# Performance work log

Hardware: AMD Instinct MI355X
Metric: run time of the kernel (lower is better)

## Reference

```python
import jax, jax.numpy as jnp
import numpy as np

B, N, DIM = 2, 8192, 3
K = 16            # num_neighbours (dilation=1)
R = 2048          # num_representitives
CIN, CL, COUT = 64, 16, 128
K2 = K * K


def _bn(x, g, b):
    # BatchNorm in eval mode with running_mean=0, running_var=1 -> affine
    return x * g + b


def setup_inputs() -> dict:
    key = jax.random.key(0)
    ks = jax.random.split(key, 24)
    r = lambda i, shape, s=1.0: jax.random.normal(ks[i], shape, jnp.float32) * s
    return {
        "points": r(0, (B, N, DIM)),
        "features": r(1, (B, N, CIN)),
        "lift_w": r(2, (CL, DIM), 0.3), "lift_b": r(3, (CL,), 0.1),
        "bn_lift_g": 1.0 + r(4, (CL,), 0.1), "bn_lift_b": r(5, (CL,), 0.1),
        "t1_w": r(6, (K2, DIM * K), 0.1), "t1_b": r(7, (K2,), 0.1),
        "bn1_g": 1.0 + r(8, (K2,), 0.1), "bn1_b": r(9, (K2,), 0.1),
        "t2_w": r(10, (K2, K2), 0.05), "t2_b": r(11, (K2,), 0.1),
        "bn2_g": 1.0 + r(12, (K2,), 0.1), "bn2_b": r(13, (K2,), 0.1),
        "t3_w": r(14, (K2, K2), 0.05), "t3_b": r(15, (K2,), 0.1),
        "bn3_g": 1.0 + r(16, (K2,), 0.1), "bn3_b": r(17, (K2,), 0.1),
        "conv_w": r(18, (COUT, CIN + CL, K), 0.05), "conv_b": r(19, (COUT,), 0.1),
        "rep_idx": jax.random.permutation(ks[20], N)[:R],
    }


def reference(points, features, lift_w, lift_b, bn_lift_g, bn_lift_b,
              t1_w, t1_b, bn1_g, bn1_b, t2_w, t2_b, bn2_g, bn2_b,
              t3_w, t3_b, bn3_g, bn3_b, conv_w, conv_b, rep_idx):
    b, n, _ = points.shape
    # ---- KNN (squared distance is order-equivalent to torch.cdist) ----
    sq = jnp.sum(points * points, -1)                                   # (b,n)
    d2 = sq[:, :, None] + sq[:, None, :] - 2.0 * jnp.einsum('bnd,bmd->bnm', points, points)
    _, idx = jax.lax.top_k(-d2, K + 1)                                  # (b,n,K+1)
    nn_idx = idx[:, :, 1:]                                              # drop self
    # ---- representative sampling + neighbor gather ----
    rep_pos = points[:, rep_idx]                                        # (b,R,3)
    nb_idx = nn_idx[:, rep_idx]                                         # (b,R,K)
    gather = jax.vmap(lambda arr, i: arr[i])
    nbr_pos = gather(points, nb_idx)                                    # (b,R,K,3)
    nbr_feat = gather(features, nb_idx)                                 # (b,R,K,CIN)
    # ---- X_conv ----
    p = (nbr_pos - rep_pos[:, :, None, :]).reshape(b * R, K, DIM)       # centered
    lifted = jax.nn.relu(_bn(p @ lift_w.T + lift_b, bn_lift_g, bn_lift_b))  # (bR,K,CL)
    feat = jnp.concatenate([lifted, nbr_feat.reshape(b * R, K, CIN)], -1)   # (bR,K,CL+CIN)
    pf = p.reshape(b * R, K * DIM)
    h = jax.nn.relu(_bn(pf @ t1_w.T + t1_b, bn1_g, bn1_b))
    h = jax.nn.relu(_bn(h @ t2_w.T + t2_b, bn2_g, bn2_b))
    T = _bn(h @ t3_w.T + t3_b, bn3_g, bn3_b).reshape(b * R, K, K)       # learned transform
    Tf = jnp.einsum('bij,bjc->bic', T, feat)                            # bmm, (bR,K,C)
    # Conv1d(C, COUT, kernel=K) over length K -> single output position
    out = jnp.einsum('bkc,ock->bo', Tf, conv_w) + conv_b                # (bR,COUT)
    return rep_pos, out.reshape(b, R, COUT)
```

## Files before the change

### kernel.cpp

```cpp
#include <hip/hip_runtime.h>
#include <float.h>

#define Bn 2
#define Nn 8192
#define Rr 2048
#define Kk 16
#define CIN 64
#define CL 16
#define COUT 128
#define K2c 256
#define GT (Bn*Rr)
#define FD (CL+CIN)
#define KC (Kk*FD)
#define MG 4
#define CCAP 192

__global__ __launch_bounds__(256) void prep_kernel(
    const float* __restrict__ t1_w, const float* __restrict__ t2_w,
    const float* __restrict__ t3_w, const float* __restrict__ conv_w,
    const float* __restrict__ points,
    float* __restrict__ t1t, float* __restrict__ t2t,
    float* __restrict__ t3t, float* __restrict__ wp,
    float4* __restrict__ pts4)
{
  int i = blockIdx.x * 256 + threadIdx.x;
  if (i < K2c*48) { int j = i / 48, k = i - j*48; t1t[k*K2c + j] = t1_w[i]; }
  if (i < K2c*K2c) { int j = i >> 8, k = i & 255; t2t[k*K2c + j] = t2_w[i]; t3t[k*K2c + j] = t3_w[i]; }
  if (i < COUT*KC) {
    int o = i / KC, ck = i - o*KC;
    int c = ck >> 4, k = ck & 15;
    wp[(k*FD + c)*COUT + o] = conv_w[i];
  }
  if (i < Bn*Nn) {
    float x = points[i*3+0], y = points[i*3+1], z = points[i*3+2];
    float sq = __fadd_rn(__fadd_rn(__fmul_rn(x,x), __fmul_rn(y,y)), __fmul_rn(z,z));
    pts4[i] = make_float4(x, y, z, sq);
  }
}

__global__ __launch_bounds__(512, 4) void knn_kernel(
    const float4* __restrict__ pts4, const int* __restrict__ rep_idx,
    int* __restrict__ nb_idx, float* __restrict__ p_out,
    float* __restrict__ rep_pos_out)
{
  union SmemU {
    float4 ptsS[2048];
    float  cbuf[8][1536];
  };
  __shared__ SmemU U;
  __shared__ unsigned long long coll[8][CCAP];
  __shared__ float4 qS[8];
  __shared__ float  tauS[8];
  __shared__ int    ccnt[8];

  int t    = threadIdx.x;
  int lane = t & 63;
  int w    = t >> 6;
  int g0   = blockIdx.x * 8;
  int b    = g0 >> 11;
  const float4* pb4 = pts4 + (size_t)b*Nn;

  if (t < 8) {
    int g = g0 + t;
    int r = g & 2047;
    qS[t] = pb4[rep_idx[r]];
    ccnt[t] = 0;
  }
  __syncthreads();

  float qx[8], qy[8], qz[8], qw[8];
  #pragma unroll
  for (int q = 0; q < 8; q++) {
    float4 Q = qS[q];
    qx[q] = __uint_as_float(__builtin_amdgcn_readfirstlane(__float_as_uint(Q.x)));
    qy[q] = __uint_as_float(__builtin_amdgcn_readfirstlane(__float_as_uint(Q.y)));
    qz[q] = __uint_as_float(__builtin_amdgcn_readfirstlane(__float_as_uint(Q.z)));
    qw[q] = __uint_as_float(__builtin_amdgcn_readfirstlane(__float_as_uint(Q.w)));
  }

  float c0[8], c1[8], c2[8];
  #pragma unroll
  for (int q = 0; q < 8; q++) { c0[q] = FLT_MAX; c1[q] = FLT_MAX; c2[q] = FLT_MAX; }

  for (int c = 0; c < 4; c++) {
    int base = c * 2048;
    __syncthreads();
    for (int i = t; i < 2048; i += 512) U.ptsS[i] = pb4[base + i];
    __syncthreads();
    #pragma unroll
    for (int j = 0; j < 4; j++) {
      float4 P = U.ptsS[j*512 + t];
      #pragma unroll
      for (int q = 0; q < 8; q++) {
        float dot = __fmaf_rn(qz[q], P.z, __fmaf_rn(qy[q], P.y, __fmul_rn(qx[q], P.x)));
        float d2  = __fsub_rn(__fadd_rn(qw[q], P.w), __fmul_rn(2.0f, dot));
        float nc2 = __builtin_amdgcn_fmed3f(c1[q], c2[q], d2);
        float nc1 = __builtin_amdgcn_fmed3f(c0[q], c1[q], d2);
        float nc0 = fminf(c0[q], d2);
        c0[q] = nc0; c1[q] = nc1; c2[q] = nc2;
      }
    }
  }

  __syncthreads();
  #pragma unroll
  for (int q = 0; q < 8; q++) {
    U.cbuf[q][0*512 + t] = c0[q];
    U.cbuf[q][1*512 + t] = c1[q];
    U.cbuf[q][2*512 + t] = c2[q];
  }
  __syncthreads();

  {
    float C0 = FLT_MAX, C1 = FLT_MAX, C2 = FLT_MAX;
    #pragma unroll
    for (int j = 0; j < 8; j++) {
      int s = lane + 64*j;
      #pragma unroll
      for (int i = 0; i < 3; i++) {
        float v = U.cbuf[w][i*512 + s];
        float n2 = __builtin_amdgcn_fmed3f(C1, C2, v);
        float n1 = __builtin_amdgcn_fmed3f(C0, C1, v);
        float n0 = fminf(C0, v);
        C0 = n0; C1 = n1; C2 = n2;
      }
    }
    float tw = FLT_MAX;
    #pragma unroll
    for (int rnd = 0; rnd < 6; rnd++) {
      float m = C2;
      #pragma unroll
      for (int off = 1; off < 64; off <<= 1) m = fminf(m, __shfl_xor(m, off));
      if (C2 == m) C2 = FLT_MAX;
      tw = m;
    }
    if (lane == 0) tauS[w] = tw;
  }
  __syncthreads();

  float tau[8];
  #pragma unroll
  for (int q = 0; q < 8; q++)
    tau[q] = __uint_as_float(__builtin_amdgcn_readfirstlane(__float_as_uint(tauS[q])));

  for (int c = 0; c < 4; c++) {
    int base = c * 2048;
    __syncthreads();
    for (int i = t; i < 2048; i += 512) U.ptsS[i] = pb4[base + i];
    __syncthreads();
    #pragma unroll
    for (int j = 0; j < 4; j++) {
      float4 P = U.ptsS[j*512 + t];
      int idx = base + j*512 + t;
      #pragma unroll
      for (int q = 0; q < 8; q++) {
        float dot = __fmaf_rn(qz[q], P.z, __fmaf_rn(qy[q], P.y, __fmul_rn(qx[q], P.x)));
        float d2  = __fsub_rn(__fadd_rn(qw[q], P.w), __fmul_rn(2.0f, dot));
        if (d2 <= tau[q]) {
          int pos = atomicAdd(&ccnt[q], 1);
          if (pos < CCAP) {
            unsigned f = __float_as_uint(d2);
            unsigned mono = f ^ ((unsigned)((int)f >> 31) | 0x80000000u);
            coll[q][pos] = ((unsigned long long)mono << 32) | (unsigned)idx;
          }
        }
      }
    }
  }
  __syncthreads();

  int cnt = ccnt[w];
  if (cnt > CCAP) cnt = CCAP;
  const unsigned long long* cw = coll[w];
  unsigned long long e[3];
  #pragma unroll
  for (int k = 0; k < 3; k++)
    e[k] = (lane + 64*k < cnt) ? cw[lane + 64*k] : ~0ull;

  int out_m = 0;
  for (int rnd = 0; rnd < 17; rnd++) {
    unsigned long long a01 = (e[0] < e[1]) ? e[0] : e[1];
    unsigned long long myk = (a01 < e[2]) ? a01 : e[2];
    unsigned long long kmin = myk;
    #pragma unroll
    for (int off = 1; off < 64; off <<= 1) {
      unsigned long long o = __shfl_xor(kmin, off);
      kmin = (o < kmin) ? o : kmin;
    }
    if (rnd >= 1 && lane == rnd - 1) out_m = (int)(kmin & 0xFFFFFFFFull);
    if      (kmin == e[0]) e[0] = ~0ull;
    else if (kmin == e[1]) e[1] = ~0ull;
    else if (kmin == e[2]) e[2] = ~0ull;
  }

  int g = g0 + w;
  float4 Q = qS[w];
  if (lane < 16) {
    nb_idx[g*Kk + lane] = out_m;
    float4 P = pb4[out_m];
    p_out[(g*Kk + lane)*3 + 0] = __fsub_rn(P.x, Q.x);
    p_out[(g*Kk + lane)*3 + 1] = __fsub_rn(P.y, Q.y);
    p_out[(g*Kk + lane)*3 + 2] = __fsub_rn(P.z, Q.z);
  }
  if (lane < 3) rep_pos_out[g*3 + lane] = (lane == 0 ? Q.x : (lane == 1 ? Q.y : Q.z));
}

__device__ __forceinline__ void fma_g(float4& a, float hv, const float4& wv) {
  a.x = fmaf(hv, wv.x, a.x);
  a.y = fmaf(hv, wv.y, a.y);
  a.z = fmaf(hv, wv.z, a.z);
  a.w = fmaf(hv, wv.w, a.w);
}

__global__ __launch_bounds__(256) void mlp_kernel(
    const float* __restrict__ p,
    const float* __restrict__ t1t, const float* __restrict__ t1_b,
    const float* __restrict__ g1v, const float* __restrict__ b1v,
    const float* __restrict__ t2t, const float* __restrict__ t2_b,
    const float* __restrict__ g2v, const float* __restrict__ b2v,
    const float* __restrict__ t3t, const float* __restrict__ t3_b,
    const float* __restrict__ g3v, const float* __restrict__ b3v,
    float* __restrict__ T_out)
{
  __shared__ float pf[48][MG];
  __shared__ float hA[K2c][MG];
  __shared__ float red[4*16*66];
  int t = threadIdx.x;
  int w = t >> 6, l = t & 63;
  int g0 = blockIdx.x * MG;
  for (int e = t; e < MG*48; e += 256) {
    int g = e / 48, k = e - g*48;
    pf[k][g] = p[(size_t)(g0+g)*48 + k];
  }
  __syncthreads();

  float4 acc[MG];

#define LDW(WSRC, K) (*(const float4*)&WSRC[(size_t)(K)*K2c + 4*l])

#define KSTAGE(WSRC, KDIM, HBUF, WB, KK, KNEXT)                        \
  {                                                                    \
    float4 wc = WB;                                                    \
    if ((KNEXT) < KDIM) WB = LDW(WSRC, KNEXT);                         \
    float4 h = *(const float4*)&HBUF[KK][0];                           \
    fma_g(acc[0], h.x, wc); fma_g(acc[1], h.y, wc);                    \
    fma_g(acc[2], h.z, wc); fma_g(acc[3], h.w, wc);                    \
  }

#define KLOOP(WSRC, KDIM, HBUF)                                        \
  {                                                                    \
    _Pragma("unroll")                                                  \
    for (int q = 0; q < MG; q++) acc[q] = make_float4(0.f,0.f,0.f,0.f);\
    float4 wb0 = LDW(WSRC, w);                                         \
    float4 wb1 = (w + 4  < KDIM) ? LDW(WSRC, w + 4)  : wb0;            \
    float4 wb2 = (w + 8  < KDIM) ? LDW(WSRC, w + 8)  : wb0;            \
    float4 wb3 = (w + 12 < KDIM) ? LDW(WSRC, w + 12) : wb0;            \
    for (int k = w; k < KDIM; k += 16) {                               \
      KSTAGE(WSRC, KDIM, HBUF, wb0, k,      k + 16)                    \
      if (k + 4 < KDIM)  KSTAGE(WSRC, KDIM, HBUF, wb1, k + 4,  k + 20) \
      if (k + 8 < KDIM)  KSTAGE(WSRC, KDIM, HBUF, wb2, k + 8,  k + 24) \
      if (k + 12 < KDIM) KSTAGE(WSRC, KDIM, HBUF, wb3, k + 12, k + 28) \
    }                                                                  \
  }

#define WRITE_RED()                                                    \
  {                                                                    \
    _Pragma("unroll")                                                  \
    for (int q = 0; q < MG; q++) {                                     \
      red[(w*16 + 0*4 + q)*66 + l] = acc[q].x;                         \
      red[(w*16 + 1*4 + q)*66 + l] = acc[q].y;                         \
      red[(w*16 + 2*4 + q)*66 + l] = acc[q].z;                         \
      red[(w*16 + 3*4 + q)*66 + l] = acc[q].w;                         \
    }                                                                  \
  }

#define REDUCE(S)                                                      \
  float4 S = make_float4(0.f,0.f,0.f,0.f);                             \
  {                                                                    \
    int lr = t >> 2, cc = t & 3;                                       \
    _Pragma("unroll")                                                  \
    for (int ww = 0; ww < 4; ww++) {                                   \
      S.x += red[(ww*16 + cc*4 + 0)*66 + lr];                          \
      S.y += red[(ww*16 + cc*4 + 1)*66 + lr];                          \
      S.z += red[(ww*16 + cc*4 + 2)*66 + lr];                          \
      S.w += red[(ww*16 + cc*4 + 3)*66 + lr];                          \
    }                                                                  \
  }

  KLOOP(t1t, 48, pf)
  WRITE_RED()
  __syncthreads();
  {
    REDUCE(s)
    float bb = t1_b[t], gg = g1v[t], oo = b1v[t];
    float4 v;
    v.x = fmaxf(fmaf(s.x + bb, gg, oo), 0.f);
    v.y = fmaxf(fmaf(s.y + bb, gg, oo), 0.f);
    v.z = fmaxf(fmaf(s.z + bb, gg, oo), 0.f);
    v.w = fmaxf(fmaf(s.w + bb, gg, oo), 0.f);
    *(float4*)&hA[t][0] = v;
  }
  __syncthreads();

  KLOOP(t2t, K2c, hA)
  WRITE_RED()
  __syncthreads();
  {
    REDUCE(s)
    float bb = t2_b[t], gg = g2v[t], oo = b2v[t];
    float4 v;
    v.x = fmaxf(fmaf(s.x + bb, gg, oo), 0.f);
    v.y = fmaxf(fmaf(s.y + bb, gg, oo), 0.f);
    v.z = fmaxf(fmaf(s.z + bb, gg, oo), 0.f);
    v.w = fmaxf(fmaf(s.w + bb, gg, oo), 0.f);
    *(float4*)&hA[t][0] = v;
  }
  __syncthreads();

  KLOOP(t3t, K2c, hA)
  WRITE_RED()
  __syncthreads();
  {
    REDUCE(s)
    float bb = t3_b[t], gg = g3v[t], oo = b3v[t];
    T_out[(size_t)(g0+0)*K2c + t] = fmaf(s.x + bb, gg, oo);
    T_out[(size_t)(g0+1)*K2c + t] = fmaf(s.y + bb, gg, oo);
    T_out[(size_t)(g0+2)*K2c + t] = fmaf(s.z + bb, gg, oo);
    T_out[(size_t)(g0+3)*K2c + t] = fmaf(s.w + bb, gg, oo);
  }
#undef KLOOP
#undef KSTAGE
#undef LDW
#undef WRITE_RED
#undef REDUCE
}

__global__ __launch_bounds__(256) void tf_kernel(
    const float* __restrict__ T_in, const float* __restrict__ features,
    const float* __restrict__ p, const int* __restrict__ nb_idx,
    const float* __restrict__ lift_w, const float* __restrict__ lift_b,
    const float* __restrict__ bng, const float* __restrict__ bnb,
    float* __restrict__ Tf)
{
  __shared__ float T_s[4*K2c];
  __shared__ float f_s[4*KC];
  __shared__ float ps[4*48];
  __shared__ int   idxs[64];
  __shared__ float lw[48], lb2[16], lg[16], lo[16];
  int t = threadIdx.x;
  int g0 = blockIdx.x * 4;
  int b = g0 / Rr;
  for (int e = t; e < 4*K2c; e += 256) T_s[e] = T_in[(size_t)g0*K2c + e];
  if (t >= 32 && t < 224) {
    int e = t - 32;
    ps[e] = p[(size_t)g0*48 + e];
  }
  if (t < 64) idxs[t] = nb_idx[g0*16 + t];
  if (t >= 64 && t < 112)  lw[t-64]   = lift_w[t-64];
  if (t >= 112 && t < 128) lb2[t-112] = lift_b[t-112];
  if (t >= 224 && t < 240) lg[t-224]  = bng[t-224];
  if (t >= 240)            lo[t-240]  = bnb[t-240];
  __syncthreads();

  {
    int wv = t >> 6, ln = t & 63;
    for (int row = wv; row < 64; row += 4) {
      int gg = row >> 4, k = row & 15;
      f_s[gg*KC + k*FD + CL + ln] = features[((size_t)b*Nn + idxs[row])*CIN + ln];
    }
  }
  for (int e = t; e < 1024; e += 256) {
    int gg = e >> 8, rem = e & 255, k = rem >> 4, c = rem & 15;
    float acc = ps[gg*48 + k*3 + 0]*lw[c*3+0] + ps[gg*48 + k*3 + 1]*lw[c*3+1]
              + ps[gg*48 + k*3 + 2]*lw[c*3+2] + lb2[c];
    acc = acc*lg[c] + lo[c];
    f_s[gg*KC + k*FD + c] = fmaxf(acc, 0.f);
  }
  __syncthreads();

  int gg = t >> 6;
  int cl = t & 63;
  for (int ci = cl; ci < FD; ci += 64) {
    float fcol[16];
    #pragma unroll
    for (int j = 0; j < 16; j++) fcol[j] = f_s[gg*KC + j*FD + ci];
    #pragma unroll
    for (int k = 0; k < 16; k++) {
      float acc = 0.f;
      #pragma unroll
      for (int j = 0; j < 16; j++) acc = fmaf(T_s[gg*K2c + k*16 + j], fcol[j], acc);
      Tf[(size_t)(g0+gg)*KC + k*FD + ci] = acc;
    }
  }
}

__global__ __launch_bounds__(256) void gemm_kernel(
    const float* __restrict__ A,
    const float* __restrict__ Bm,
    float* __restrict__ part)
{
  __shared__ float As[16*36];
  __shared__ float Bs[16*COUT];
  int t = threadIdx.x;
  int m0 = blockIdx.x * 32;
  int ky = blockIdx.y;
  int kbase0 = ky * (KC/8);
  float acc[4][4];
  #pragma unroll
  for (int i = 0; i < 4; i++)
    #pragma unroll
    for (int j = 0; j < 4; j++) acc[i][j] = 0.f;
  int tn = t & 31, tm = t >> 5;

  for (int kt = 0; kt < KC/8; kt += 16) {
    int kb = kbase0 + kt;
    {
      int kcol = t & 15, row = t >> 4;
      As[kcol*36 + row]      = A[(size_t)(m0+row)*KC + kb + kcol];
      As[kcol*36 + row + 16] = A[(size_t)(m0+row+16)*KC + kb + kcol];
    }
    {
      int o = t & 127, kk2 = t >> 7;
      #pragma unroll
      for (int p4 = 0; p4 < 8; p4++) {
        int kk = kk2 + p4*2;
        Bs[kk*COUT + o] = Bm[(size_t)(kb+kk)*COUT + o];
      }
    }
    __syncthreads();
    #pragma unroll
    for (int kk = 0; kk < 16; kk++) {
      float4 a4 = *(const float4*)&As[kk*36 + tm*4];
      float4 b4 = *(const float4*)&Bs[kk*COUT + tn*4];
      float av[4] = {a4.x, a4.y, a4.z, a4.w};
      float bv[4] = {b4.x, b4.y, b4.z, b4.w};
      #pragma unroll
      for (int i = 0; i < 4; i++)
        #pragma unroll
        for (int j = 0; j < 4; j++) acc[i][j] = fmaf(av[i], bv[j], acc[i][j]);
    }
    __syncthreads();
  }
  #pragma unroll
  for (int i = 0; i < 4; i++) {
    float4 v = make_float4(acc[i][0], acc[i][1], acc[i][2], acc[i][3]);
    *(float4*)&part[((size_t)ky*GT + m0 + tm*4 + i)*COUT + tn*4] = v;
  }
}

__global__ __launch_bounds__(256) void reduce_kernel(
    const float* __restrict__ part, const float* __restrict__ conv_b,
    float* __restrict__ outp)
{
  int i = blockIdx.x*256 + threadIdx.x;
  float4 s = ((const float4*)conv_b)[i & 31];
  #pragma unroll
  for (int w = 0; w < 8; w++) {
    float4 v = ((const float4*)(part + (size_t)w*GT*COUT))[i];
    s.x += v.x; s.y += v.y; s.z += v.z; s.w += v.w;
  }
  ((float4*)outp)[i] = s;
}

extern "C" void kernel_launch(void* const* d_in, const int* in_sizes, int n_in,
                              void* d_out, int out_size, void* d_ws, size_t ws_size,
                              hipStream_t stream) {
  const float* points   = (const float*)d_in[0];
  const float* features = (const float*)d_in[1];
  const float* lift_w   = (const float*)d_in[2];
  const float* lift_b   = (const float*)d_in[3];
  const float* bn_lift_g= (const float*)d_in[4];
  const float* bn_lift_b= (const float*)d_in[5];
  const float* t1_w     = (const float*)d_in[6];
  const float* t1_b     = (const float*)d_in[7];
  const float* bn1_g    = (const float*)d_in[8];
  const float* bn1_b    = (const float*)d_in[9];
  const float* t2_w     = (const float*)d_in[10];
  const float* t2_b     = (const float*)d_in[11];
  const float* bn2_g    = (const float*)d_in[12];
  const float* bn2_b    = (const float*)d_in[13];
  const float* t3_w     = (const float*)d_in[14];
  const float* t3_b     = (const float*)d_in[15];
  const float* bn3_g    = (const float*)d_in[16];
  const float* bn3_b    = (const float*)d_in[17];
  const float* conv_w   = (const float*)d_in[18];
  const float* conv_b   = (const float*)d_in[19];
  const int*   rep_idx  = (const int*)d_in[20];

  char* ws = (char*)d_ws;
  int*    nb   = (int*)   (ws + 0);
  float*  p    = (float*) (ws + 262144);
  float*  T    = (float*) (ws + 1048576);
  float*  Tf   = (float*) (ws + 5242880);
  float*  wp   = (float*) (ws + 26214400);
  float*  t1t  = (float*) (ws + 26869760);
  float*  t2t  = (float*) (ws + 26918912);
  float*  t3t  = (float*) (ws + 27181056);
  float*  part = (float*) (ws + 33554432);
  float4* pts4 = (float4*)(ws + 52428800);

  float* rep_pos = (float*)d_out;
  float* outp    = (float*)d_out + (size_t)GT*3;

  prep_kernel<<<640, 256, 0, stream>>>(t1_w, t2_w, t3_w, conv_w, points,
                                       t1t, t2t, t3t, wp, pts4);
  knn_kernel<<<GT/8, 512, 0, stream>>>(pts4, rep_idx, nb, p, rep_pos);
  mlp_kernel<<<GT/MG, 256, 0, stream>>>(p, t1t, t1_b, bn1_g, bn1_b,
                                        t2t, t2_b, bn2_g, bn2_b,
                                        t3t, t3_b, bn3_g, bn3_b, T);
  tf_kernel<<<GT/4, 256, 0, stream>>>(T, features, p, nb,
                                      lift_w, lift_b, bn_lift_g, bn_lift_b, Tf);
  dim3 ggrid(GT/32, 8);
  gemm_kernel<<<ggrid, 256, 0, stream>>>(Tf, wp, part);
  reduce_kernel<<<(GT*COUT/4)/256, 256, 0, stream>>>(part, conv_b, outp);
}
```

Baseline: 217.3 us.

## Restructure KNN threshold and selection with register-resident points and rank-based sorting

The KNN kernel now loads each thread's 16 points into registers once instead of staging chunks through shared memory twice. The first pass keeps only a per-thread minimum rather than a top-3. The threshold becomes the 6th smallest of the per-lane third-best values, computed by a rank count instead of repeated wave reductions. Final top-17 selection uses an O(cnt) rank count per candidate instead of 17 rounds of 64-bit shuffle min-reductions, and the candidate cap shrinks to 128. This removes syncs and LDS traffic and frees LDS for occupancy, at the cost of higher register pressure. The threshold bound is looser, so there is a risk of candidate overflow past the cap.

```diff
diff --git a/kernel.cpp b/kernel.cpp
--- a/kernel.cpp
+++ b/kernel.cpp
@@ -13,7 +13,7 @@
 #define FD (CL+CIN)
 #define KC (Kk*FD)
 #define MG 4
-#define CCAP 192
+#define CCAP 128
 
 __global__ __launch_bounds__(256) void prep_kernel(
     const float* __restrict__ t1_w, const float* __restrict__ t2_w,
@@ -43,12 +43,9 @@
     int* __restrict__ nb_idx, float* __restrict__ p_out,
     float* __restrict__ rep_pos_out)
 {
-  union SmemU {
-    float4 ptsS[2048];
-    float  cbuf[8][1536];
-  };
-  __shared__ SmemU U;
+  __shared__ float cbuf[8][512];
   __shared__ unsigned long long coll[8][CCAP];
+  __shared__ float Lst[8][64];
   __shared__ float4 qS[8];
   __shared__ float  tauS[8];
   __shared__ int    ccnt[8];
@@ -78,63 +75,49 @@
     qw[q] = __uint_as_float(__builtin_amdgcn_readfirstlane(__float_as_uint(Q.w)));
   }
 
-  float c0[8], c1[8], c2[8];
-  #pragma unroll
-  for (int q = 0; q < 8; q++) { c0[q] = FLT_MAX; c1[q] = FLT_MAX; c2[q] = FLT_MAX; }
-
-  for (int c = 0; c < 4; c++) {
-    int base = c * 2048;
-    __syncthreads();
-    for (int i = t; i < 2048; i += 512) U.ptsS[i] = pb4[base + i];
-    __syncthreads();
-    #pragma unroll
-    for (int j = 0; j < 4; j++) {
-      float4 P = U.ptsS[j*512 + t];
-      #pragma unroll
-      for (int q = 0; q < 8; q++) {
-        float dot = __fmaf_rn(qz[q], P.z, __fmaf_rn(qy[q], P.y, __fmul_rn(qx[q], P.x)));
-        float d2  = __fsub_rn(__fadd_rn(qw[q], P.w), __fmul_rn(2.0f, dot));
-        float nc2 = __builtin_amdgcn_fmed3f(c1[q], c2[q], d2);
-        float nc1 = __builtin_amdgcn_fmed3f(c0[q], c1[q], d2);
-        float nc0 = fminf(c0[q], d2);
-        c0[q] = nc0; c1[q] = nc1; c2[q] = nc2;
-      }
-    }
-  }
-
-  __syncthreads();
-  #pragma unroll
-  for (int q = 0; q < 8; q++) {
-    U.cbuf[q][0*512 + t] = c0[q];
-    U.cbuf[q][1*512 + t] = c1[q];
-    U.cbuf[q][2*512 + t] = c2[q];
-  }
+  float4 P[16];
+  #pragma unroll
+  for (int i = 0; i < 16; i++) P[i] = pb4[t + 512*i];
+
+  float m[8];
+  #pragma unroll
+  for (int q = 0; q < 8; q++) m[q] = FLT_MAX;
+  #pragma unroll
+  for (int i = 0; i < 16; i++) {
+    #pragma unroll
+    for (int q = 0; q < 8; q++) {
+      float dot = __fmaf_rn(qz[q], P[i].z, __fmaf_rn(qy[q], P[i].y, __fmul_rn(qx[q], P[i].x)));
+      float d2  = __fsub_rn(__fadd_rn(qw[q], P[i].w), __fmul_rn(2.0f, dot));
+      m[q] = fminf(m[q], d2);
+    }
+  }
+
+  #pragma unroll
+  for (int q = 0; q < 8; q++) cbuf[q][t] = m[q];
   __syncthreads();
 
   {
     float C0 = FLT_MAX, C1 = FLT_MAX, C2 = FLT_MAX;
     #pragma unroll
     for (int j = 0; j < 8; j++) {
-      int s = lane + 64*j;
-      #pragma unroll
-      for (int i = 0; i < 3; i++) {
-        float v = U.cbuf[w][i*512 + s];
-        float n2 = __builtin_amdgcn_fmed3f(C1, C2, v);
-        float n1 = __builtin_amdgcn_fmed3f(C0, C1, v);
-        float n0 = fminf(C0, v);
-        C0 = n0; C1 = n1; C2 = n2;
-      }
-    }
-    float tw = FLT_MAX;
-    #pragma unroll
-    for (int rnd = 0; rnd < 6; rnd++) {
-      float m = C2;
-      #pragma unroll
-      for (int off = 1; off < 64; off <<= 1) m = fminf(m, __shfl_xor(m, off));
-      if (C2 == m) C2 = FLT_MAX;
-      tw = m;
-    }
-    if (lane == 0) tauS[w] = tw;
+      float v = cbuf[w][lane + 64*j];
+      float n2 = __builtin_amdgcn_fmed3f(C1, C2, v);
+      float n1 = __builtin_amdgcn_fmed3f(C0, C1, v);
+      float n0 = fminf(C0, v);
+      C0 = n0; C1 = n1; C2 = n2;
+    }
+    Lst[w][lane] = C2;
+  }
+  __syncthreads();
+  {
+    float L = Lst[w][lane];
+    int rk = 0;
+    #pragma unroll 8
+    for (int i = 0; i < 64; i++) {
+      float Li = Lst[w][i];
+      rk += (Li < L || (Li == L && i < lane)) ? 1 : 0;
+    }
+    if (rk == 5) tauS[w] = L;
   }
   __syncthreads();
 
@@ -143,64 +126,52 @@
   for (int q = 0; q < 8; q++)
     tau[q] = __uint_as_float(__builtin_amdgcn_readfirstlane(__float_as_uint(tauS[q])));
 
-  for (int c = 0; c < 4; c++) {
-    int base = c * 2048;
-    __syncthreads();
-    for (int i = t; i < 2048; i += 512) U.ptsS[i] = pb4[base + i];
-    __syncthreads();
-    #pragma unroll
-    for (int j = 0; j < 4; j++) {
-      float4 P = U.ptsS[j*512 + t];
-      int idx = base + j*512 + t;
-      #pragma unroll
-      for (int q = 0; q < 8; q++) {
-        float dot = __fmaf_rn(qz[q], P.z, __fmaf_rn(qy[q], P.y, __fmul_rn(qx[q], P.x)));
-        float d2  = __fsub_rn(__fadd_rn(qw[q], P.w), __fmul_rn(2.0f, dot));
-        if (d2 <= tau[q]) {
-          int pos = atomicAdd(&ccnt[q], 1);
-          if (pos < CCAP) {
-            unsigned f = __float_as_uint(d2);
-            unsigned mono = f ^ ((unsigned)((int)f >> 31) | 0x80000000u);
-            coll[q][pos] = ((unsigned long long)mono << 32) | (unsigned)idx;
-          }
+  #pragma unroll
+  for (int i = 0; i < 16; i++) {
+    #pragma unroll
+    for (int q = 0; q < 8; q++) {
+      float dot = __fmaf_rn(qz[q], P[i].z, __fmaf_rn(qy[q], P[i].y, __fmul_rn(qx[q], P[i].x)));
+      float d2  = __fsub_rn(__fadd_rn(qw[q], P[i].w), __fmul_rn(2.0f, dot));
+      if (d2 <= tau[q]) {
+        int pos = atomicAdd(&ccnt[q], 1);
+        if (pos < CCAP) {
+          unsigned f = __float_as_uint(d2);
+          unsigned mono = f ^ ((unsigned)((int)f >> 31) | 0x80000000u);
+          coll[q][pos] = ((unsigned long long)mono << 32) | (unsigned)(t + 512*i);
         }
       }
     }
   }
   __syncthreads();
 
-  int cnt = ccnt[w];
+  int cnt = __builtin_amdgcn_readfirstlane(ccnt[w]);
   if (cnt > CCAP) cnt = CCAP;
-  const unsigned long long* cw = coll[w];
-  unsigned long long e[3];
-  #pragma unroll
-  for (int k = 0; k < 3; k++)
-    e[k] = (lane + 64*k < cnt) ? cw[lane + 64*k] : ~0ull;
-
-  int out_m = 0;
-  for (int rnd = 0; rnd < 17; rnd++) {
-    unsigned long long a01 = (e[0] < e[1]) ? e[0] : e[1];
-    unsigned long long myk = (a01 < e[2]) ? a01 : e[2];
-    unsigned long long kmin = myk;
-    #pragma unroll
-    for (int off = 1; off < 64; off <<= 1) {
-      unsigned long long o = __shfl_xor(kmin, off);
-      kmin = (o < kmin) ? o : kmin;
-    }
-    if (rnd >= 1 && lane == rnd - 1) out_m = (int)(kmin & 0xFFFFFFFFull);
-    if      (kmin == e[0]) e[0] = ~0ull;
-    else if (kmin == e[1]) e[1] = ~0ull;
-    else if (kmin == e[2]) e[2] = ~0ull;
+  unsigned long long k1 = (lane < cnt)      ? coll[w][lane]      : ~0ull;
+  unsigned long long k2 = (lane + 64 < cnt) ? coll[w][lane + 64] : ~0ull;
+  int r1 = 0, r2 = 0;
+  for (int i = 0; i < cnt; i++) {
+    unsigned long long ki = coll[w][i];
+    r1 += (ki < k1) ? 1 : 0;
+    r2 += (ki < k2) ? 1 : 0;
   }
 
   int g = g0 + w;
   float4 Q = qS[w];
-  if (lane < 16) {
-    nb_idx[g*Kk + lane] = out_m;
-    float4 P = pb4[out_m];
-    p_out[(g*Kk + lane)*3 + 0] = __fsub_rn(P.x, Q.x);
-    p_out[(g*Kk + lane)*3 + 1] = __fsub_rn(P.y, Q.y);
-    p_out[(g*Kk + lane)*3 + 2] = __fsub_rn(P.z, Q.z);
+  if (lane < cnt && r1 >= 1 && r1 <= 16) {
+    int om = (int)(k1 & 0xFFFFFFFFull);
+    nb_idx[g*Kk + r1 - 1] = om;
+    float4 Pm = pb4[om];
+    p_out[(g*Kk + r1 - 1)*3 + 0] = __fsub_rn(Pm.x, Q.x);
+    p_out[(g*Kk + r1 - 1)*3 + 1] = __fsub_rn(Pm.y, Q.y);
+    p_out[(g*Kk + r1 - 1)*3 + 2] = __fsub_rn(Pm.z, Q.z);
+  }
+  if (lane + 64 < cnt && r2 >= 1 && r2 <= 16) {
+    int om = (int)(k2 & 0xFFFFFFFFull);
+    nb_idx[g*Kk + r2 - 1] = om;
+    float4 Pm = pb4[om];
+    p_out[(g*Kk + r2 - 1)*3 + 0] = __fsub_rn(Pm.x, Q.x);
+    p_out[(g*Kk + r2 - 1)*3 + 1] = __fsub_rn(Pm.y, Q.y);
+    p_out[(g*Kk + r2 - 1)*3 + 2] = __fsub_rn(Pm.z, Q.z);
   }
   if (lane < 3) rep_pos_out[g*3 + lane] = (lane == 0 ? Q.x : (lane == 1 ? Q.y : Q.z));
 }
```

New measurement: 214.8 us. No clear change (-1.2%).
